# Kernel optimization log

Measured on AMD Instinct MI355X. Metric: run time of the kernel, lower is better.

## Reference

```python
import jax, jax.numpy as jnp
import numpy as np

B, C, H, W = 4, 256, 48, 48
HEADS, DH = 8, 32
INNER = HEADS * DH
HID = 128  # max(16, INNER//2)
SCALE = DH ** -0.5
EPS = 1e-6


def setup_inputs() -> dict:
    key = jax.random.key(0)
    ks = jax.random.split(key, 32)
    s = 0.02
    inp = {
        'x': jax.random.normal(ks[0], (B, C, H, W), jnp.float32),
        'rgb_input': jax.random.uniform(ks[1], (B, 3, H, W), jnp.float32),
        'wq': jax.random.normal(ks[2], (INNER, C), jnp.float32) * s,
        'bq': jnp.zeros((INNER,), jnp.float32),
        'wk': jax.random.normal(ks[3], (INNER, C), jnp.float32) * s,
        'bk': jnp.zeros((INNER,), jnp.float32),
        'wv': jax.random.normal(ks[4], (INNER, C), jnp.float32) * s,
        'bv': jnp.zeros((INNER,), jnp.float32),
        'wproj': jax.random.normal(ks[5], (C, INNER), jnp.float32) * s,
        'bproj': jnp.zeros((C,), jnp.float32),
        'c1_w': jax.random.normal(ks[6], (HID, 1, 3, 3), jnp.float32) * s,
        'c1_b': jnp.zeros((HID,), jnp.float32),
        'c2_w': jax.random.normal(ks[7], (HID, HID, 3, 3), jnp.float32) * s,
        'c2_b': jnp.zeros((HID,), jnp.float32),
        'gq_w': jax.random.normal(ks[8], (INNER, HID), jnp.float32) * s,
        'gq_b': jnp.ones((INNER,), jnp.float32),
        'bqf_w': jax.random.normal(ks[9], (INNER, HID), jnp.float32) * s,
        'bqf_b': jnp.zeros((INNER,), jnp.float32),
        'gk_w': jax.random.normal(ks[10], (INNER, HID), jnp.float32) * s,
        'gk_b': jnp.ones((INNER,), jnp.float32),
        'bkf_w': jax.random.normal(ks[11], (INNER, HID), jnp.float32) * s,
        'bkf_b': jnp.zeros((INNER,), jnp.float32),
        'gv_w': jax.random.normal(ks[12], (INNER, HID), jnp.float32) * s,
        'gv_b': jnp.ones((INNER,), jnp.float32),
        'bvf_w': jax.random.normal(ks[13], (INNER, HID), jnp.float32) * s,
        'bvf_b': jnp.zeros((INNER,), jnp.float32),
        'alpha': jnp.float32(0.1),
    }
    return inp


def _conv3(x, w, b):
    y = jax.lax.conv_general_dilated(x, w, (1, 1), 'SAME',
                                     dimension_numbers=('NCHW', 'OIHW', 'NCHW'))
    return y + b[None, :, None, None]


def _rgb_to_luma(rgb):
    y = 0.299 * rgb[:, 0:1] + 0.587 * rgb[:, 1:2] + 0.114 * rgb[:, 2:3]
    y_min = jnp.min(y, axis=(2, 3), keepdims=True)
    y_max = jnp.max(y, axis=(2, 3), keepdims=True)
    return (y - y_min) / (y_max - y_min + EPS)


def reference(x, rgb_input, wq, bq, wk, bk, wv, bv, wproj, bproj,
              c1_w, c1_b, c2_w, c2_b,
              gq_w, gq_b, bqf_w, bqf_b, gk_w, gk_b, bkf_w, bkf_b,
              gv_w, gv_b, bvf_w, bvf_b, alpha):
    Bx, Cx, Hx, Wx = x.shape
    N = Hx * Wx
    luma = _rgb_to_luma(rgb_input)  # [B,1,H,W]

    # LumaCond trunk + FiLM params (1x1 convs then global spatial mean)
    h = jax.nn.relu(_conv3(luma, c1_w, c1_b))
    h = jax.nn.relu(_conv3(h, c2_w, c2_b))
    hm = h.mean(axis=(2, 3))  # [B,HID] (mean commutes with 1x1 conv)

    def film_params(gw, gb, bw, bb):
        g = hm @ gw.T + gb  # [B, INNER]
        bta = hm @ bw.T + bb
        return (g.reshape(Bx, HEADS, DH, 1), bta.reshape(Bx, HEADS, DH, 1))

    gq, fbq = film_params(gq_w, gq_b, bqf_w, bqf_b)
    gk, fbk = film_params(gk_w, gk_b, bkf_w, bkf_b)
    gv, fbv = film_params(gv_w, gv_b, bvf_w, bvf_b)

    def proj_film(w, b, g, bta):
        t = jnp.einsum('bchw,oc->bohw', x, w) + b[None, :, None, None]
        t = t.reshape(Bx, HEADS, DH, N)
        return g * t + bta  # [B,heads,dh,N]

    q = proj_film(wq, bq, gq, fbq)
    k = proj_film(wk, bk, gk, fbk)
    v = proj_film(wv, bv, gv, fbv)

    logits = jnp.einsum('bhdn,bhdm->bhnm', q, k) * SCALE  # [B,heads,N,N]

    # luma bias: avg-pooled inverse luma, mean-centered per image
    invL = 1.0 - luma
    invL = jax.lax.reduce_window(invL, 0.0, jax.lax.add,
                                 (1, 1, 3, 3), (1, 1, 1, 1), 'SAME') / 9.0
    invL = invL.reshape(Bx, N)
    invL = invL - invL.mean(axis=-1, keepdims=True)
    logits = logits + alpha * invL[:, None, None, :]

    attn = jax.nn.softmax(logits, axis=-1)
    out = jnp.einsum('bhnm,bhdm->bhdn', attn, v)  # [B,heads,dh,N]
    out = out.reshape(Bx, INNER, Hx, Wx)
    return jnp.einsum('bchw,oc->bohw', out, wproj) + bproj[None, :, None, None]
```

## Files before the change

kernel.cpp:

```cpp
#include <hip/hip_runtime.h>


#define NSP 2304
#define WID 48

typedef __attribute__((ext_vector_type(4))) float  fvec4;
typedef __attribute__((ext_vector_type(2))) unsigned int uvec2;
typedef __attribute__((ext_vector_type(4))) unsigned int uvec4;
typedef __attribute__((ext_vector_type(8))) short  short8;
typedef __attribute__((ext_vector_type(4))) float  f32x4;

__device__ inline unsigned short f2bf(float f){
  unsigned int u = __builtin_bit_cast(unsigned int, f);
  u += 0x7fffu + ((u >> 16) & 1u);
  return (unsigned short)(u >> 16);
}
__device__ inline unsigned pack2bf(float a, float b){
#if __has_builtin(__builtin_amdgcn_cvt_pk_bf16_f32)
  typedef __attribute__((ext_vector_type(2))) __bf16 bf16x2;
  bf16x2 r = __builtin_amdgcn_cvt_pk_bf16_f32(a, b);
  return __builtin_bit_cast(unsigned, r);
#else
  return (unsigned)f2bf(a) | ((unsigned)f2bf(b) << 16);
#endif
}

__global__ void k0b_wcast(const float* __restrict__ c2w, const float* __restrict__ wq,
                          const float* __restrict__ wk, const float* __restrict__ wv_,
                          const float* __restrict__ wproj,
                          unsigned short* __restrict__ wtb,
                          unsigned short* __restrict__ wqkvb,
                          unsigned short* __restrict__ wprojb){
  int idx = blockIdx.x*256 + threadIdx.x;
  if (idx < 147456){
    int ic = idx & 127, rem = idx >> 7;
    int oc = rem & 127, tap = rem >> 7;
    wtb[idx] = f2bf(c2w[(oc*128 + ic)*9 + tap]);
  } else if (idx < 344064){
    int j = idx - 147456;
    int mat = j >> 16, oc_ = j & 65535;
    const float* src = (mat == 0) ? wq : (mat == 1) ? wk : wv_;
    wqkvb[j] = f2bf(src[oc_]);
  } else {
    int j = idx - 344064;
    wprojb[j] = f2bf(wproj[j]);
  }
}

__global__ __launch_bounds__(256) void k0xt(const float* __restrict__ x,
                                            unsigned short* __restrict__ xt){
  int nt = blockIdx.x, cc = blockIdx.y, b = blockIdx.z, t = threadIdx.x;
  __shared__ unsigned short tb[64*72];
  int cl0 = t >> 4;
  int nl0 = (t & 15) * 4;
  #pragma unroll
  for (int ps = 0; ps < 4; ++ps){
    int cl = cl0 + ps*16;
    fvec4 v = *(const fvec4*)(x + ((size_t)(b*256 + cc*64 + cl))*NSP + nt*64 + nl0);
    #pragma unroll
    for (int i = 0; i < 4; ++i) tb[(nl0+i)*72 + cl] = f2bf(v[i]);
  }
  __syncthreads();
  int nl = t >> 2, cg = (t & 3) * 16;
  uvec4 u0 = *(const uvec4*)&tb[nl*72 + cg];
  uvec4 u1 = *(const uvec4*)&tb[nl*72 + cg + 8];
  unsigned short* dst = xt + ((size_t)(b*NSP + nt*64 + nl))*256 + cc*64 + cg;
  *(uvec4*)dst = u0;
  *(uvec4*)(dst + 8) = u1;
}

__global__ void k1_luma(const float* __restrict__ rgb, const float* __restrict__ alphaP,
                        float* __restrict__ luma_n, float* __restrict__ bias_a,
                        float* __restrict__ hm_sum){
  int b = blockIdx.x, t = threadIdx.x;
  __shared__ float ly[NSP];
  __shared__ float ll[NSP];
  __shared__ float red[256];
  __shared__ float red2[256];
  const float* rp = rgb + b*3*NSP;
  float lmin = 1e30f, lmax = -1e30f;
  for (int i = t; i < NSP; i += 256){
    float y = 0.299f*rp[i] + 0.587f*rp[NSP+i] + 0.114f*rp[2*NSP+i];
    ly[i] = y; lmin = fminf(lmin, y); lmax = fmaxf(lmax, y);
  }
  red[t] = lmin; red2[t] = lmax;
  __syncthreads();
  for (int s = 128; s > 0; s >>= 1){
    if (t < s){ red[t] = fminf(red[t], red[t+s]); red2[t] = fmaxf(red2[t], red2[t+s]); }
    __syncthreads();
  }
  float mn = red[0], mx = red2[0];
  float inv = 1.0f / (mx - mn + 1e-6f);
  for (int i = t; i < NSP; i += 256){
    float v = (ly[i] - mn) * inv;
    ll[i] = v;
    luma_n[b*NSP + i] = v;
  }
  if (t < 128) hm_sum[b*128 + t] = 0.f;
  __syncthreads();
  float pr[9]; float psum = 0.f;
  #pragma unroll
  for (int ii = 0; ii < 9; ++ii){
    int n = t + 256*ii;
    int row = n / WID, col = n - row*WID;
    float s = 0.f;
    #pragma unroll
    for (int dy = -1; dy <= 1; ++dy)
      #pragma unroll
      for (int dx = -1; dx <= 1; ++dx){
        int r2 = row+dy, c2 = col+dx;
        if (r2 >= 0 && r2 < WID && c2 >= 0 && c2 < WID) s += 1.0f - ll[r2*WID + c2];
      }
    pr[ii] = s * (1.f/9.f);
    psum += pr[ii];
  }
  __syncthreads();
  red[t] = psum;
  __syncthreads();
  for (int s = 128; s > 0; s >>= 1){
    if (t < s) red[t] += red[t+s];
    __syncthreads();
  }
  float mean = red[0] * (1.f/(float)NSP);
  float alpha = alphaP[0] * 1.4426950408889634f;
  #pragma unroll
  for (int ii = 0; ii < 9; ++ii){
    int n = t + 256*ii;
    bias_a[b*NSP + n] = alpha * (pr[ii] - mean);
  }
}

__global__ void k2_conv1(const float* __restrict__ luma_n, const float* __restrict__ c1w,
                         const float* __restrict__ c1b, unsigned short* __restrict__ h1p){
  int nt = blockIdx.x, ocg = blockIdx.y, b = blockIdx.z, t = threadIdx.x;
  __shared__ float wsm[32*9];
  __shared__ float bsm[32];
  for (int i = t; i < 288; i += 256) wsm[i] = c1w[ocg*288 + i];
  if (t < 32) bsm[t] = c1b[ocg*32 + t];
  __syncthreads();
  int n = nt*256 + t;
  int row = n / WID, col = n - row*WID;
  const float* lp = luma_n + b*NSP;
  float lv[9];
  int k = 0;
  #pragma unroll
  for (int dy = -1; dy <= 1; ++dy)
    #pragma unroll
    for (int dx = -1; dx <= 1; ++dx, ++k){
      int r2 = row+dy, c2 = col+dx;
      lv[k] = (r2 >= 0 && r2 < WID && c2 >= 0 && c2 < WID) ? lp[r2*WID + c2] : 0.f;
    }
  unsigned int packed[16];
  #pragma unroll
  for (int oc2 = 0; oc2 < 16; ++oc2){
    float a0 = bsm[oc2*2], a1 = bsm[oc2*2+1];
    #pragma unroll
    for (int q = 0; q < 9; ++q){
      a0 += wsm[(oc2*2)*9 + q] * lv[q];
      a1 += wsm[(oc2*2+1)*9 + q] * lv[q];
    }
    packed[oc2] = pack2bf(fmaxf(a0, 0.f), fmaxf(a1, 0.f));
  }
  unsigned short* dst = h1p + ((size_t)(b*2500 + (row+1)*50 + (col+1)))*128 + ocg*32;
  #pragma unroll
  for (int q4 = 0; q4 < 4; ++q4)
    *(uvec4*)(dst + q4*8) = *(uvec4*)&packed[q4*4];
}

__global__ __launch_bounds__(256) void k3_conv2(const unsigned short* __restrict__ h1p,
    const unsigned short* __restrict__ wtb, const float* __restrict__ c2b,
    float* __restrict__ hm_sum){
  int row = blockIdx.x, mh = blockIdx.y, b = blockIdx.z;
  int t = threadIdx.x, wv = t >> 6, lane = t & 63;
  int lq = lane >> 4, lc = lane & 15;
  int ocb = mh*64 + wv*16;
  const f32x4 z4 = {0.f, 0.f, 0.f, 0.f};
  f32x4 C[3] = {z4, z4, z4};
  const unsigned short* hbase = h1p + (size_t)b*2500*128;
  #pragma unroll
  for (int tap = 0; tap < 9; ++tap){
    int dy = tap/3 - 1, dx = tap%3 - 1;
    const unsigned short* wrow = wtb + (tap*128 + ocb + lc)*128 + lq*8;
    const unsigned short* hrow = hbase + ((row+dy+1)*50 + (dx+1) + lc)*128 + lq*8;
    #pragma unroll
    for (int kc = 0; kc < 4; ++kc){
      short8 aW = *(const short8*)(wrow + kc*32);
      #pragma unroll
      for (int ntp = 0; ntp < 3; ++ntp){
        short8 bH = *(const short8*)(hrow + ntp*16*128 + kc*32);
        C[ntp] = __builtin_amdgcn_mfma_f32_16x16x32_bf16(aW, bH, C[ntp], 0, 0, 0);
      }
    }
  }
  float s[4];
  #pragma unroll
  for (int r = 0; r < 4; ++r){
    float bias = c2b[ocb + lq*4 + r];
    float v = 0.f;
    #pragma unroll
    for (int ntp = 0; ntp < 3; ++ntp) v += fmaxf(C[ntp][r] + bias, 0.f);
    v += __shfl_xor(v, 1, 64);
    v += __shfl_xor(v, 2, 64);
    v += __shfl_xor(v, 4, 64);
    v += __shfl_xor(v, 8, 64);
    s[r] = v;
  }
  if (lc == 0){
    #pragma unroll
    for (int r = 0; r < 4; ++r)
      atomicAdd(&hm_sum[b*128 + ocb + lq*4 + r], s[r]);
  }
}

__global__ void k4_film(const float* __restrict__ hm_sum,
  const float* w0, const float* b0, const float* w1, const float* b1,
  const float* w2, const float* b2, const float* w3, const float* b3,
  const float* w4, const float* b4, const float* w5, const float* b5,
  float* __restrict__ film){
  __shared__ float hs[128];
  int bb = blockIdx.x & 3, m6 = blockIdx.x >> 2, t = threadIdx.x;
  if (t < 128) hs[t] = hm_sum[bb*128 + t] * (1.f/(float)NSP);
  __syncthreads();
  const float* wm[6] = {w0,w1,w2,w3,w4,w5};
  const float* bm[6] = {b0,b1,b2,b3,b4,b5};
  const float* w = wm[m6];
  int o = t;
  float a = bm[m6][o];
  for (int h2 = 0; h2 < 128; ++h2) a += hs[h2] * w[o*128 + h2];
  film[blockIdx.x*256 + t] = a;
}

__global__ __launch_bounds__(256) void k5_qkv(const unsigned short* __restrict__ xt,
    const unsigned short* __restrict__ wqkvb,
    const float* __restrict__ bq, const float* __restrict__ bk, const float* __restrict__ bv,
    const float* __restrict__ film,
    unsigned short* __restrict__ q_t, unsigned short* __restrict__ k_t,
    unsigned short* __restrict__ v_b){
  int nt = blockIdx.x, ot = blockIdx.y, b = blockIdx.z;
  int t = threadIdx.x, wv = t >> 6, lane = t & 63;
  int lq = lane >> 4, lc = lane & 15;
  int p = ot >> 1;
  int omb = (ot & 1)*128 + wv*32;
  const unsigned short* wb = wqkvb + p*65536;
  const f32x4 z4 = {0.f, 0.f, 0.f, 0.f};
  f32x4 acc[2][4];
  #pragma unroll
  for (int oh = 0; oh < 2; ++oh)
    #pragma unroll
    for (int nq = 0; nq < 4; ++nq) acc[oh][nq] = z4;
  for (int kc = 0; kc < 8; ++kc){
    short8 aW[2];
    #pragma unroll
    for (int oh = 0; oh < 2; ++oh)
      aW[oh] = *(const short8*)(wb + (omb + oh*16 + lc)*256 + kc*32 + lq*8);
    short8 bX[4];
    #pragma unroll
    for (int nq = 0; nq < 4; ++nq)
      bX[nq] = *(const short8*)(xt + ((size_t)(b*NSP + nt*64 + nq*16 + lc))*256 + kc*32 + lq*8);
    #pragma unroll
    for (int oh = 0; oh < 2; ++oh)
      #pragma unroll
      for (int nq = 0; nq < 4; ++nq)
        acc[oh][nq] = __builtin_amdgcn_mfma_f32_16x16x32_bf16(aW[oh], bX[nq], acc[oh][nq], 0, 0, 0);
  }
  const float* bvec = (p == 0) ? bq : (p == 1) ? bk : bv;
  int hq = omb >> 5;
  unsigned short* qk = (p == 0) ? q_t : k_t;
  #pragma unroll
  for (int oh = 0; oh < 2; ++oh){
    fvec4 g4 = *(const fvec4*)(film + (2*p*4 + b)*256 + omb + oh*16 + lq*4);
    fvec4 t4 = *(const fvec4*)(film + ((2*p+1)*4 + b)*256 + omb + oh*16 + lq*4);
    fvec4 z4b = *(const fvec4*)(bvec + omb + oh*16 + lq*4);
    #pragma unroll
    for (int nq = 0; nq < 4; ++nq){
      int n = nt*64 + nq*16 + lc;
      float v0 = g4[0]*(acc[oh][nq][0] + z4b[0]) + t4[0];
      float v1 = g4[1]*(acc[oh][nq][1] + z4b[1]) + t4[1];
      float v2 = g4[2]*(acc[oh][nq][2] + z4b[2]) + t4[2];
      float v3 = g4[3]*(acc[oh][nq][3] + z4b[3]) + t4[3];
      if (p == 0){
        const float sc = 0.17677669529663687f * 1.4426950408889634f;
        v0 *= sc; v1 *= sc; v2 *= sc; v3 *= sc;
      }
      if (p < 2){
        uvec2 u;
        u.x = pack2bf(v0, v1);
        u.y = pack2bf(v2, v3);
        *(uvec2*)(qk + ((size_t)((b*8 + hq)*NSP + n))*32 + oh*16 + lq*4) = u;
      } else {
        int om = omb + oh*16 + lq*4;
        v_b[((size_t)(b*256 + om + 0))*NSP + n] = f2bf(v0);
        v_b[((size_t)(b*256 + om + 1))*NSP + n] = f2bf(v1);
        v_b[((size_t)(b*256 + om + 2))*NSP + n] = f2bf(v2);
        v_b[((size_t)(b*256 + om + 3))*NSP + n] = f2bf(v3);
      }
    }
  }
}

__global__ __launch_bounds__(256) void k6_attn(const unsigned short* __restrict__ q_t,
    const unsigned short* __restrict__ k_t, const unsigned short* __restrict__ v_b,
    const float* __restrict__ bias_a,
    unsigned short* __restrict__ o0, unsigned short* __restrict__ o1,
    float* __restrict__ l0, float* __restrict__ l1){
  int bx = blockIdx.x, h = blockIdx.y, b = blockIdx.z;
  int qblk = bx >> 1, s = bx & 1;
  unsigned short* op = s ? o1 : o0;
  float* lp = s ? l1 : l0;
  int t = threadIdx.x, wv = t >> 6, lane = t & 63;
  int lq = lane >> 4, lc = lane & 15;
  int bh = b*8 + h;
  int nb0 = qblk*128 + wv*32;
  const f32x4 z4 = {0.f, 0.f, 0.f, 0.f};
  __shared__ float ps[4][512];
  float* myps = ps[wv];
  int xm = (lc & 7) << 2;
  int wbase = lc*32;
  const uvec4 onesu = {0x3F803F80u, 0x3F803F80u, 0x3F803F80u, 0x3F803F80u};
  const short8 aOnes = __builtin_bit_cast(short8, onesu);
  short8 aQ[2];
  #pragma unroll
  for (int qf = 0; qf < 2; ++qf)
    aQ[qf] = *(const short8*)(q_t + ((size_t)(bh*NSP + nb0 + qf*16 + lc))*32 + lq*8);
  f32x4 O[2][2];
  f32x4 Ol[2];
  #pragma unroll
  for (int qf = 0; qf < 2; ++qf){
    Ol[qf] = z4;
    #pragma unroll
    for (int dh = 0; dh < 2; ++dh) O[qf][dh] = z4;
  }
  const float* brow = bias_a + b*NSP;
  int ms = s*1152;

  for (int it = 0; it < 18; ++it){
    int m0 = ms + it*64;
    short8 aK[4]; fvec4 c0[4]; short8 aV[2][2];
    #pragma unroll
    for (int g = 0; g < 4; ++g)
      aK[g] = *(const short8*)(k_t + ((size_t)(bh*NSP + m0 + g*16 + lc))*32 + lq*8);
    #pragma unroll
    for (int g = 0; g < 4; ++g)
      c0[g] = *(const fvec4*)(brow + m0 + g*16 + lq*4);
    #pragma unroll
    for (int dh = 0; dh < 2; ++dh)
      #pragma unroll
      for (int mh = 0; mh < 2; ++mh)
        aV[dh][mh] = *(const short8*)(v_b + ((size_t)(b*256 + h*32 + dh*16 + lc))*NSP + m0 + mh*32 + lq*8);
    #pragma unroll
    for (int qf = 0; qf < 2; ++qf){
      #pragma unroll
      for (int g = 0; g < 4; ++g){
        f32x4 S = __builtin_amdgcn_mfma_f32_16x16x32_bf16(aK[g], aQ[qf], c0[g], 0, 0, 0);
        uvec2 w2;
        w2.x = pack2bf(__builtin_amdgcn_exp2f(S[0]), __builtin_amdgcn_exp2f(S[1]));
        w2.y = pack2bf(__builtin_amdgcn_exp2f(S[2]), __builtin_amdgcn_exp2f(S[3]));
        int kp = g*8 + lq*2;
        *(uvec2*)&myps[wbase + (kp ^ xm)] = w2;
      }
      #pragma unroll
      for (int mh = 0; mh < 2; ++mh){
        int rb = (mh*16 + lq*4) ^ xm;
        uvec4 up = *(const uvec4*)&myps[wbase + rb];
        short8 bP = __builtin_bit_cast(short8, up);
        Ol[qf] = __builtin_amdgcn_mfma_f32_16x16x32_bf16(aOnes, bP, Ol[qf], 0, 0, 0);
        #pragma unroll
        for (int dh = 0; dh < 2; ++dh)
          O[qf][dh] = __builtin_amdgcn_mfma_f32_16x16x32_bf16(aV[dh][mh], bP, O[qf][dh], 0, 0, 0);
      }
    }
  }
  #pragma unroll
  for (int qf = 0; qf < 2; ++qf){
    int nidx = nb0 + qf*16 + lc;
    if (lq == 0) lp[b*NSP + nidx] = Ol[qf][0];
    #pragma unroll
    for (int dh = 0; dh < 2; ++dh){
      uvec2 u;
      u.x = pack2bf(O[qf][dh][0], O[qf][dh][1]);
      u.y = pack2bf(O[qf][dh][2], O[qf][dh][3]);
      *(uvec2*)(op + ((size_t)(b*NSP + nidx))*256 + h*32 + dh*16 + lq*4) = u;
    }
  }
}

__global__ __launch_bounds__(256) void k7_proj(const unsigned short* __restrict__ a0,
    const unsigned short* __restrict__ a1, const float* __restrict__ l0p,
    const float* __restrict__ l1p, const unsigned short* __restrict__ wprojb,
    const float* __restrict__ bproj, float* __restrict__ out){
  int nt = blockIdx.x, ct = blockIdx.y, b = blockIdx.z;
  int t = threadIdx.x, wv = t >> 6, lane = t & 63;
  int lq = lane >> 4, lc = lane & 15;
  __shared__ float rls[32];
  if (t < 32) rls[t] = 1.0f / (l0p[b*NSP + nt*32 + t] + l1p[b*NSP + nt*32 + t]);
  __syncthreads();
  int cb = ct*128 + wv*32;
  const f32x4 z4 = {0.f, 0.f, 0.f, 0.f};
  f32x4 acc[2][2];
  #pragma unroll
  for (int ch = 0; ch < 2; ++ch)
    #pragma unroll
    for (int nq = 0; nq < 2; ++nq) acc[ch][nq] = z4;
  for (int kc = 0; kc < 8; ++kc){
    short8 aW[2];
    #pragma unroll
    for (int ch = 0; ch < 2; ++ch)
      aW[ch] = *(const short8*)(wprojb + (cb + ch*16 + lc)*256 + kc*32 + lq*8);
    #pragma unroll
    for (int src = 0; src < 2; ++src){
      const unsigned short* ap = src ? a1 : a0;
      short8 bA[2];
      #pragma unroll
      for (int nq = 0; nq < 2; ++nq)
        bA[nq] = *(const short8*)(ap + ((size_t)(b*NSP + nt*32 + nq*16 + lc))*256 + kc*32 + lq*8);
      #pragma unroll
      for (int ch = 0; ch < 2; ++ch)
        #pragma unroll
        for (int nq = 0; nq < 2; ++nq)
          acc[ch][nq] = __builtin_amdgcn_mfma_f32_16x16x32_bf16(aW[ch], bA[nq], acc[ch][nq], 0, 0, 0);
    }
  }
  #pragma unroll
  for (int ch = 0; ch < 2; ++ch){
    #pragma unroll
    for (int nq = 0; nq < 2; ++nq){
      int n = nt*32 + nq*16 + lc;
      float rl = rls[nq*16 + lc];
      #pragma unroll
      for (int r = 0; r < 4; ++r){
        int c = cb + ch*16 + lq*4 + r;
        out[((size_t)(b*256 + c))*NSP + n] = acc[ch][nq][r]*rl + bproj[c];
      }
    }
  }
}

extern "C" void kernel_launch(void* const* d_in, const int* in_sizes, int n_in,
                              void* d_out, int out_size, void* d_ws, size_t ws_size,
                              hipStream_t stream) {
  const float* x     = (const float*)d_in[0];
  const float* rgb   = (const float*)d_in[1];
  const float* wq    = (const float*)d_in[2];
  const float* bq    = (const float*)d_in[3];
  const float* wk    = (const float*)d_in[4];
  const float* bk    = (const float*)d_in[5];
  const float* wv    = (const float*)d_in[6];
  const float* bv    = (const float*)d_in[7];
  const float* wproj = (const float*)d_in[8];
  const float* bproj = (const float*)d_in[9];
  const float* c1w   = (const float*)d_in[10];
  const float* c1b   = (const float*)d_in[11];
  const float* c2w   = (const float*)d_in[12];
  const float* c2b   = (const float*)d_in[13];
  const float* gq_w  = (const float*)d_in[14];
  const float* gq_b  = (const float*)d_in[15];
  const float* bqf_w = (const float*)d_in[16];
  const float* bqf_b = (const float*)d_in[17];
  const float* gk_w  = (const float*)d_in[18];
  const float* gk_b  = (const float*)d_in[19];
  const float* bkf_w = (const float*)d_in[20];
  const float* bkf_b = (const float*)d_in[21];
  const float* gv_w  = (const float*)d_in[22];
  const float* gv_b  = (const float*)d_in[23];
  const float* bvf_w = (const float*)d_in[24];
  const float* bvf_b = (const float*)d_in[25];
  const float* alphaP= (const float*)d_in[26];

  char* w = (char*)d_ws;
  float* luma_n = (float*)w;            w += 4*NSP*4;
  float* bias_a = (float*)w;            w += 4*NSP*4;
  float* hm_sum = (float*)w;            w += 512*4;
  float* film   = (float*)w;            w += 6*4*256*4;
  unsigned short* h1p = (unsigned short*)w; w += 4*2500*128*2;
  unsigned short* wtb = (unsigned short*)w; w += 9*128*128*2;
  unsigned short* wqkvb = (unsigned short*)w; w += 3*256*256*2;
  unsigned short* wprojb = (unsigned short*)w; w += 256*256*2;
  unsigned short* xt  = (unsigned short*)w; w += (size_t)4*NSP*256*2;
  unsigned short* q_t = (unsigned short*)w; w += (size_t)4*8*NSP*32*2;
  unsigned short* k_t = (unsigned short*)w; w += (size_t)4*8*NSP*32*2;
  unsigned short* v_b = (unsigned short*)w; w += (size_t)4*256*NSP*2;
  unsigned short* o_part0 = (unsigned short*)w; w += (size_t)4*NSP*256*2;
  unsigned short* o_part1 = (unsigned short*)w; w += (size_t)4*NSP*256*2;
  float* l_part0 = (float*)w;           w += 4*NSP*4;
  float* l_part1 = (float*)w;           w += 4*NSP*4;

  (void)hipMemsetAsync(h1p, 0, (size_t)4*2500*128*2, stream);
  k0b_wcast<<<1600, 256, 0, stream>>>(c2w, wq, wk, wv, wproj, wtb, wqkvb, wprojb);
  k0xt    <<<dim3(36,4,4), 256, 0, stream>>>(x, xt);
  k1_luma <<<4, 256, 0, stream>>>(rgb, alphaP, luma_n, bias_a, hm_sum);
  k2_conv1<<<dim3(9,4,4), 256, 0, stream>>>(luma_n, c1w, c1b, h1p);
  k3_conv2<<<dim3(48,2,4), 256, 0, stream>>>(h1p, wtb, c2b, hm_sum);
  k4_film <<<24, 256, 0, stream>>>(hm_sum, gq_w, gq_b, bqf_w, bqf_b,
                                   gk_w, gk_b, bkf_w, bkf_b,
                                   gv_w, gv_b, bvf_w, bvf_b, film);
  k5_qkv  <<<dim3(36,6,4), 256, 0, stream>>>(xt, wqkvb, bq, bk, bv, film,
                                             q_t, k_t, v_b);
  k6_attn <<<dim3(36,8,4), 256, 0, stream>>>(q_t, k_t, v_b, bias_a,
                                             o_part0, o_part1, l_part0, l_part1);
  k7_proj <<<dim3(72,2,4), 256, 0, stream>>>(o_part0, o_part1, l_part0, l_part1,
                                             wprojb, bproj, (float*)d_out);
}
```

Before: 295.3 us.

## Stage K/V tiles through double-buffered LDS with register prefetch in attention kernel

```diff
diff --git a/kernel.cpp b/kernel.cpp
--- a/kernel.cpp
+++ b/kernel.cpp
@@ -298,7 +298,7 @@
   }
 }
 
-__global__ __launch_bounds__(256) void k6_attn(const unsigned short* __restrict__ q_t,
+__global__ __launch_bounds__(256, 4) void k6_attn(const unsigned short* __restrict__ q_t,
     const unsigned short* __restrict__ k_t, const unsigned short* __restrict__ v_b,
     const float* __restrict__ bias_a,
     unsigned short* __restrict__ o0, unsigned short* __restrict__ o1,
@@ -312,63 +312,99 @@
   int bh = b*8 + h;
   int nb0 = qblk*128 + wv*32;
   const f32x4 z4 = {0.f, 0.f, 0.f, 0.f};
-  __shared__ float ps[4][512];
-  float* myps = ps[wv];
-  int xm = (lc & 7) << 2;
+  int ms = s*1152;
+
+  __shared__ unsigned short Kb[2][64*32];
+  __shared__ unsigned short Vb[2][32*64];
+  __shared__ float ps[4][1024];
+
+  const unsigned short* kg = k_t + ((size_t)bh*NSP + ms + (t>>2))*32 + (t&3)*8;
+  const unsigned short* vg = v_b + ((size_t)(b*256 + h*32 + (t>>3)))*NSP + ms + (t&7)*8;
+  int krow = t >> 2;
+  unsigned short* kw = &Kb[0][krow*32 + (((t&3) ^ ((krow>>1)&3))*8)];
+  int vrow = t >> 3;
+  unsigned short* vw = &Vb[0][vrow*64 + (((t&7) ^ (vrow&7))*8)];
+
+  int kcol = (lq ^ ((lc>>1)&3))*8;
+  int sxm = ((lc&7)<<2) | (((lc>>3)&1)<<1);
   int wbase = lc*32;
+
+  const float* brow = bias_a + b*NSP + ms;
+  fvec4 c0r[4];
+  #pragma unroll
+  for (int g = 0; g < 4; ++g) c0r[g] = *(const fvec4*)(brow + g*16 + lq*4);
+
+  short8 aQ[2];
+  #pragma unroll
+  for (int qf = 0; qf < 2; ++qf)
+    aQ[qf] = *(const short8*)(q_t + ((size_t)(bh*NSP + nb0 + qf*16 + lc))*32 + lq*8);
+
+  uvec4 gKr = *(const uvec4*)kg;
+  uvec4 gVr = *(const uvec4*)vg;
+
   const uvec4 onesu = {0x3F803F80u, 0x3F803F80u, 0x3F803F80u, 0x3F803F80u};
   const short8 aOnes = __builtin_bit_cast(short8, onesu);
-  short8 aQ[2];
-  #pragma unroll
-  for (int qf = 0; qf < 2; ++qf)
-    aQ[qf] = *(const short8*)(q_t + ((size_t)(bh*NSP + nb0 + qf*16 + lc))*32 + lq*8);
-  f32x4 O[2][2];
-  f32x4 Ol[2];
+
+  f32x4 O[2][2]; f32x4 Ol[2];
   #pragma unroll
   for (int qf = 0; qf < 2; ++qf){
-    Ol[qf] = z4;
-    #pragma unroll
-    for (int dh = 0; dh < 2; ++dh) O[qf][dh] = z4;
-  }
-  const float* brow = bias_a + b*NSP;
-  int ms = s*1152;
+    Ol[qf] = z4; O[qf][0] = z4; O[qf][1] = z4;
+  }
+  float* myps = ps[wv];
 
   for (int it = 0; it < 18; ++it){
-    int m0 = ms + it*64;
-    short8 aK[4]; fvec4 c0[4]; short8 aV[2][2];
+    int buf = it & 1;
+    *(uvec4*)(kw + buf*2048) = gKr;
+    *(uvec4*)(vw + buf*2048) = gVr;
+    __syncthreads();
+    if (it < 17){
+      gKr = *(const uvec4*)(kg + (it+1)*2048);
+      gVr = *(const uvec4*)(vg + (it+1)*64);
+    }
+    const unsigned short* kb = Kb[buf];
+    const unsigned short* vb = Vb[buf];
+    short8 aK[4], aV[2][2];
     #pragma unroll
     for (int g = 0; g < 4; ++g)
-      aK[g] = *(const short8*)(k_t + ((size_t)(bh*NSP + m0 + g*16 + lc))*32 + lq*8);
-    #pragma unroll
-    for (int g = 0; g < 4; ++g)
-      c0[g] = *(const fvec4*)(brow + m0 + g*16 + lq*4);
-    #pragma unroll
-    for (int dh = 0; dh < 2; ++dh)
+      aK[g] = *(const short8*)(kb + (g*16 + lc)*32 + kcol);
+    #pragma unroll
+    for (int dhg = 0; dhg < 2; ++dhg)
       #pragma unroll
       for (int mh = 0; mh < 2; ++mh)
-        aV[dh][mh] = *(const short8*)(v_b + ((size_t)(b*256 + h*32 + dh*16 + lc))*NSP + m0 + mh*32 + lq*8);
+        aV[dhg][mh] = *(const short8*)(vb + (dhg*16 + lc)*64 + (((mh*4 + lq) ^ (lc&7))*8));
     #pragma unroll
     for (int qf = 0; qf < 2; ++qf){
       #pragma unroll
       for (int g = 0; g < 4; ++g){
-        f32x4 S = __builtin_amdgcn_mfma_f32_16x16x32_bf16(aK[g], aQ[qf], c0[g], 0, 0, 0);
+        f32x4 S = __builtin_amdgcn_mfma_f32_16x16x32_bf16(aK[g], aQ[qf], c0r[g], 0, 0, 0);
         uvec2 w2;
         w2.x = pack2bf(__builtin_amdgcn_exp2f(S[0]), __builtin_amdgcn_exp2f(S[1]));
         w2.y = pack2bf(__builtin_amdgcn_exp2f(S[2]), __builtin_amdgcn_exp2f(S[3]));
-        int kp = g*8 + lq*2;
-        *(uvec2*)&myps[wbase + (kp ^ xm)] = w2;
-      }
+        *(uvec2*)&myps[qf*512 + wbase + ((g*8 + lq*2) ^ sxm)] = w2;
+      }
+    }
+    if (it < 17){
+      #pragma unroll
+      for (int g = 0; g < 4; ++g)
+        c0r[g] = *(const fvec4*)(brow + (it+1)*64 + g*16 + lq*4);
+    }
+    __builtin_amdgcn_s_setprio(1);
+    #pragma unroll
+    for (int qf = 0; qf < 2; ++qf){
       #pragma unroll
       for (int mh = 0; mh < 2; ++mh){
-        int rb = (mh*16 + lq*4) ^ xm;
-        uvec4 up = *(const uvec4*)&myps[wbase + rb];
+        int d0 = (mh*16 + lq*4) ^ sxm;
+        uvec2 lo = *(const uvec2*)&myps[qf*512 + wbase + d0];
+        uvec2 hi = *(const uvec2*)&myps[qf*512 + wbase + (d0 ^ 2)];
+        uvec4 up; up.x = lo.x; up.y = lo.y; up.z = hi.x; up.w = hi.y;
         short8 bP = __builtin_bit_cast(short8, up);
         Ol[qf] = __builtin_amdgcn_mfma_f32_16x16x32_bf16(aOnes, bP, Ol[qf], 0, 0, 0);
         #pragma unroll
-        for (int dh = 0; dh < 2; ++dh)
-          O[qf][dh] = __builtin_amdgcn_mfma_f32_16x16x32_bf16(aV[dh][mh], bP, O[qf][dh], 0, 0, 0);
-      }
-    }
+        for (int dhg = 0; dhg < 2; ++dhg)
+          O[qf][dhg] = __builtin_amdgcn_mfma_f32_16x16x32_bf16(aV[dhg][mh], bP, O[qf][dhg], 0, 0, 0);
+      }
+    }
+    __builtin_amdgcn_s_setprio(0);
   }
   #pragma unroll
   for (int qf = 0; qf < 2; ++qf){
```

New measurement: 267.5 us. -9.4%, faster.
